# Kernel optimization log

Measured on AMD Instinct MI355X. Metric: run time of the kernel, lower is better.

## Reference

```python
import jax, jax.numpy as jnp
import numpy as np

N_CLASSES = 40
EMBED_DIM = 128
MOMENTUM = 0.1
LAMBDA_R, LAMBDA_C, LAMBDA_M = 1.0, 0.5, 1.0
BATCH = 262144


def setup_inputs() -> dict:
    key = jax.random.key(0)
    k1, k2, k3 = jax.random.split(key, 3)
    z = jax.random.normal(k1, (BATCH, EMBED_DIM), dtype=jnp.float32)
    y = jax.random.randint(k2, (BATCH,), 0, N_CLASSES)
    centers = jax.random.normal(k3, (N_CLASSES, EMBED_DIM), dtype=jnp.float32)
    initialized = jnp.ones((N_CLASSES,), dtype=bool)
    # buffers derived from class_counts (imbalanced ramp), r0=gamma=m0=1, alpha=0.25
    counts = jnp.asarray([1000.0 * (i + 1) for i in range(N_CLASSES)], jnp.float32)
    n_max = jnp.max(counts)
    target_radii = 1.0 + 1.0 * jnp.log(n_max / (counts + 1.0))
    margins = 1.0 * jnp.power(n_max / (counts + 1.0), 0.25)
    return {"z": z, "y": y, "centers": centers, "initialized": initialized,
            "target_radii": target_radii, "margins": margins}


def _update_centers(z, y, centers, initialized):
    # EMA centroid update on detached embeddings (torch.no_grad equivalent).
    zs = jax.lax.stop_gradient(z)
    sums = jax.ops.segment_sum(zs, y, num_segments=N_CLASSES)            # [C, D]
    cnt = jax.ops.segment_sum(jnp.ones((zs.shape[0],), zs.dtype), y,
                              num_segments=N_CLASSES)                    # [C]
    mean = sums / jnp.maximum(cnt, 1.0)[:, None]
    ema = (1.0 - MOMENTUM) * centers + MOMENTUM * mean
    new = jnp.where(initialized[:, None], ema, mean)                     # first-touch init
    return jnp.where((cnt > 0)[:, None], new, centers)                   # skip empty classes


def reference(z, y, centers, initialized, target_radii, margins):
    c = _update_centers(z, y, centers, initialized)                      # [C, D]

    # radial loss: smooth L1 (beta=1) between ||z|| and per-class target radius
    r = jnp.linalg.norm(z, axis=-1)                                      # [B]
    d = r - target_radii[y]
    ad = jnp.abs(d)
    loss_radial = jnp.mean(jnp.where(ad < 1.0, 0.5 * d * d, ad - 0.5))

    # compact loss: mean squared distance to own centroid
    diff = z - c[y]                                                      # [B, D]
    loss_compact = jnp.mean(jnp.sum(diff * diff, axis=-1))

    # margin loss: min distance to any other class centroid via Gram trick
    z2 = jnp.sum(z * z, axis=-1)                                         # [B]
    c2 = jnp.sum(c * c, axis=-1)                                         # [C]
    d2 = z2[:, None] + c2[None, :] - 2.0 * (z @ c.T)                     # [B, C]
    dist = jnp.sqrt(jnp.maximum(d2, 0.0))
    own = y[:, None] == jnp.arange(N_CLASSES)[None, :]                   # [B, C] bool
    dist_opp = jnp.min(jnp.where(own, jnp.inf, dist), axis=1)            # [B]
    loss_margin = jnp.mean(jax.nn.relu(margins[y] - dist_opp))

    return LAMBDA_R * loss_radial + LAMBDA_C * loss_compact + LAMBDA_M * loss_margin
```

## Files before the change

kernel.cpp:

```cpp
#include <hip/hip_runtime.h>
#include <math.h>

#define BATCH 262144
#define DIM   128
#define NCLS  40
#define NCP   48
#define CD    (NCLS * DIM)

#define TB1 512
#define NB1 256
#define TB3 256
#define NB3 (BATCH / 256)

typedef __attribute__((ext_vector_type(8))) short short8;
typedef __attribute__((ext_vector_type(4))) float f32x4;

__device__ __forceinline__ short f2bf(float f) {
    unsigned u = __float_as_uint(f);
    u += 0x7fffu + ((u >> 16) & 1u);
    return (short)(u >> 16);
}

#define K1_ALL(M) M(0) M(1) M(2) M(3) M(4) M(5) M(6) M(7) M(8) M(9) \
                  M(10) M(11) M(12) M(13) M(14) M(15) M(16) M(17) M(18) M(19) \
                  M(20) M(21) M(22) M(23) M(24) M(25) M(26) M(27) M(28) M(29) \
                  M(30) M(31) M(32) M(33) M(34) M(35) M(36) M(37) M(38) M(39)
#define K1_DECL(c) float a##c = 0.0f;
#define K1_CASE(c) case c: a##c += v; break;
#define K1_ST(c)   s_acc[w][(c) * 64 + lane] = a##c;

__global__ __launch_bounds__(TB1) void k1_segsum(const float* __restrict__ z,
                                                 const int* __restrict__ y,
                                                 float* __restrict__ ps,
                                                 float* __restrict__ gcnt) {
    __shared__ float s_acc[8][NCLS * 64];
    __shared__ float s_cnt[NCLS];
    const int t = threadIdx.x;
    if (t < NCLS) s_cnt[t] = 0.0f;
    __syncthreads();

    const int w    = t >> 6;
    const int lane = t & 63;
    const int p    = w >> 1;
    const int h    = w & 1;
    const int base = blockIdx.x * 1024;

    int yy[4];
#pragma unroll
    for (int g = 0; g < 4; ++g) yy[g] = y[base + 4 * (g * 64 + lane) + p];

    if (h == 0) {
#pragma unroll
        for (int g = 0; g < 4; ++g) atomicAdd(&s_cnt[yy[g]], 1.0f);
    }

    const float* __restrict__ zp = z + (size_t)base * DIM + h * 64 + lane;

    float vb[8];
#pragma unroll
    for (int q = 0; q < 8; ++q) vb[q] = zp[(size_t)(4 * q + p) * DIM];

    K1_ALL(K1_DECL)

#pragma unroll 1
    for (int g = 0; g < 4; ++g) {
        const int yg = yy[g];
#pragma unroll 1
        for (int j0 = 0; j0 < 64; j0 += 8) {
#pragma unroll
            for (int q = 0; q < 8; ++q) {
                const int sj = g * 64 + j0 + q;
                const float v = vb[q];
                int sn = sj + 8;
                if (sn > 255) sn = sj;
                vb[q] = zp[(size_t)(4 * sn + p) * DIM];
                const int cls = __builtin_amdgcn_readlane(yg, j0 + q);
                switch (cls) { K1_ALL(K1_CASE) default: break; }
            }
        }
    }

    K1_ALL(K1_ST)
    __syncthreads();

    float* __restrict__ ps_b = ps + (size_t)blockIdx.x * CD;
    for (int i = t; i < CD; i += TB1) {
        const int cls = i >> 7;
        const int d   = i & 127;
        const int hh  = d >> 6, dl = d & 63;
        float ssum = 0.0f;
#pragma unroll
        for (int pp = 0; pp < 4; ++pp) ssum += s_acc[(pp << 1) | hh][cls * 64 + dl];
        ps_b[i] = ssum;
    }
    if (t < NCLS) atomicAdd(&gcnt[t], s_cnt[t]);
}

__global__ __launch_bounds__(512) void k2_centers(const float* __restrict__ part_sums,
                                                  const float* __restrict__ gcnt,
                                                  const float* __restrict__ centers,
                                                  short* __restrict__ cbf,
                                                  float* __restrict__ c2_out) {
    const int j  = blockIdx.x;
    const int t  = threadIdx.x;
    const int d  = t & 127;
    const int qr = t >> 7;

    if (j >= NCLS) {
        if (qr == 0) cbf[j * DIM + d] = 0;
        if (t == 0) c2_out[j] = 1e30f;
        return;
    }

    const float* __restrict__ p = part_sums + j * DIM + d + (size_t)(qr * 64) * CD;
    float s = 0.0f;
#pragma unroll 8
    for (int b = 0; b < 64; ++b) s += p[(size_t)b * CD];

    __shared__ float red[512];
    red[t] = s;
    __syncthreads();

    float cv = 0.0f;
    if (qr == 0) {
        const float ssum = red[d] + red[d + 128] + red[d + 256] + red[d + 384];
        const float cnt  = gcnt[j];
        const float mean = ssum / fmaxf(cnt, 1.0f);
        const float ctr  = centers[j * DIM + d];
        const float ema  = 0.9f * ctr + 0.1f * mean;
        cv = (cnt > 0.0f) ? ema : ctr;
        cbf[j * DIM + d] = f2bf(cv);
    }
    __syncthreads();
    red[t] = cv * cv;
    __syncthreads();
    for (int off = 256; off > 0; off >>= 1) {
        if (t < off) red[t] += red[t + off];
        __syncthreads();
    }
    if (t == 0) c2_out[j] = red[0];
}

__global__ __launch_bounds__(TB3) void k3_loss(const float* __restrict__ z,
                                               const int* __restrict__ y,
                                               const short* __restrict__ cbf,
                                               const float* __restrict__ c2,
                                               const float* __restrict__ tr,
                                               const float* __restrict__ mg,
                                               float* __restrict__ out) {
    __shared__ float s_S[4][64 * 52];
    __shared__ float s_c2[NCP];

    const int t = threadIdx.x;
    if (t < NCP) s_c2[t] = c2[t];

    const int w    = t >> 6;
    const int lane = t & 63;
    const int q    = lane >> 4;
    const int col  = lane & 15;
    const int wavebase = blockIdx.x * 256 + w * 64;

    short8 bfrag[3][4];
#pragma unroll
    for (int ct = 0; ct < 3; ++ct)
#pragma unroll
        for (int s = 0; s < 4; ++s)
            bfrag[ct][s] = *(const short8*)(cbf + (ct * 16 + col) * DIM + s * 32 + q * 8);

    __syncthreads();

#pragma unroll 1
    for (int rt = 0; rt < 4; ++rt) {
        const float* __restrict__ zrow =
            z + (size_t)(wavebase + rt * 16 + col) * DIM + q * 8;

        float4 f[8];
#pragma unroll
        for (int s = 0; s < 4; ++s) {
            f[2 * s]     = *(const float4*)(zrow + s * 32);
            f[2 * s + 1] = *(const float4*)(zrow + s * 32 + 4);
        }

        float zp = 0.0f;
#pragma unroll
        for (int i = 0; i < 8; ++i) {
            zp = fmaf(f[i].x, f[i].x, zp);
            zp = fmaf(f[i].y, f[i].y, zp);
            zp = fmaf(f[i].z, f[i].z, zp);
            zp = fmaf(f[i].w, f[i].w, zp);
        }

        short8 afr[4];
#pragma unroll
        for (int s = 0; s < 4; ++s) {
            const float4 f0 = f[2 * s], f1 = f[2 * s + 1];
            afr[s][0] = f2bf(f0.x); afr[s][1] = f2bf(f0.y);
            afr[s][2] = f2bf(f0.z); afr[s][3] = f2bf(f0.w);
            afr[s][4] = f2bf(f1.x); afr[s][5] = f2bf(f1.y);
            afr[s][6] = f2bf(f1.z); afr[s][7] = f2bf(f1.w);
        }

        f32x4 acc0 = {0.f, 0.f, 0.f, 0.f};
        f32x4 acc1 = {0.f, 0.f, 0.f, 0.f};
        f32x4 acc2 = {0.f, 0.f, 0.f, 0.f};
#pragma unroll
        for (int s = 0; s < 4; ++s) {
            acc0 = __builtin_amdgcn_mfma_f32_16x16x32_bf16(afr[s], bfrag[0][s], acc0, 0, 0, 0);
            acc1 = __builtin_amdgcn_mfma_f32_16x16x32_bf16(afr[s], bfrag[1][s], acc1, 0, 0, 0);
            acc2 = __builtin_amdgcn_mfma_f32_16x16x32_bf16(afr[s], bfrag[2][s], acc2, 0, 0, 0);
        }

        zp += __shfl_xor(zp, 16);
        zp += __shfl_xor(zp, 32);
        if (q == 0) s_S[w][(rt * 16 + col) * 52 + 48] = zp;

#pragma unroll
        for (int reg = 0; reg < 4; ++reg) {
            const int rr = rt * 16 + q * 4 + reg;
            s_S[w][rr * 52 + col]      = acc0[reg];
            s_S[w][rr * 52 + 16 + col] = acc1[reg];
            s_S[w][rr * 52 + 32 + col] = acc2[reg];
        }
    }

    const int row = blockIdx.x * 256 + t;
    const int cls = y[row];
    const float z2v = s_S[w][lane * 52 + 48];

    float own_d2 = 0.0f;
    float mind2  = 3.4e38f;
#pragma unroll
    for (int k = 0; k < 12; ++k) {
        const float4 Sv = *(const float4*)&s_S[w][lane * 52 + 4 * k];
        const float Se[4] = {Sv.x, Sv.y, Sv.z, Sv.w};
#pragma unroll
        for (int e = 0; e < 4; ++e) {
            const int j = 4 * k + e;
            float d2 = fmaxf(z2v + s_c2[j] - 2.0f * Se[e], 0.0f);
            const bool isown = (j == cls);
            own_d2 = isown ? d2 : own_d2;
            mind2  = isown ? mind2 : fminf(mind2, d2);
        }
    }

    const float r  = sqrtf(z2v);
    const float dd = r - tr[cls];
    const float ad = fabsf(dd);
    const float rad = (ad < 1.0f) ? 0.5f * dd * dd : ad - 0.5f;

    const float dist = sqrtf(mind2);
    const float marg = fmaxf(mg[cls] - dist, 0.0f);

    const float tot = rad + 0.5f * own_d2 + marg;

    __syncthreads();
    float* s_red = &s_S[0][0];
    s_red[t] = tot;
    __syncthreads();
    for (int off = TB3 / 2; off > 0; off >>= 1) {
        if (t < off) s_red[t] += s_red[t + off];
        __syncthreads();
    }
    if (t == 0) atomicAdd(out, s_red[0] * (1.0f / (float)BATCH));
}

extern "C" void kernel_launch(void* const* d_in, const int* in_sizes, int n_in,
                              void* d_out, int out_size, void* d_ws, size_t ws_size,
                              hipStream_t stream) {
    const float* z       = (const float*)d_in[0];
    const int*   y       = (const int*)d_in[1];
    const float* centers = (const float*)d_in[2];
    const float* tr      = (const float*)d_in[4];
    const float* mg      = (const float*)d_in[5];
    float* out = (float*)d_out;

    float* ws        = (float*)d_ws;
    float* part_sums = ws;
    float* c2buf     = part_sums + (size_t)NB1 * CD;
    float* gcnt      = c2buf + NCP;
    short* cbf       = (short*)(gcnt + NCLS);

    hipMemsetAsync(gcnt, 0, NCLS * sizeof(float), stream);
    hipMemsetAsync(out, 0, sizeof(float), stream);

    k1_segsum<<<NB1, TB1, 0, stream>>>(z, y, part_sums, gcnt);
    k2_centers<<<NCP, 512, 0, stream>>>(part_sums, gcnt, centers, cbf, c2buf);
    k3_loss<<<NB3, TB3, 0, stream>>>(z, y, cbf, c2buf, tr, mg, out);
}
```

Measured before the change: 264.8 us.

## Restructure segment-sum kernel to 4 waves with float2 per-lane accumulators

The segment-sum kernel now uses 256 threads (4 waves) per block instead of 512. Each lane covers two adjacent dimensions with float2 loads and float2 register accumulators over 40 classes, and each wave walks 256 contiguous rows. The 8-slab shared-memory reduction is replaced by a single shared buffer that the waves accumulate into one after another, separated by barriers. The aim is to cut shared memory use and the final reduction cost, with wider coalesced loads. In exchange it doubles per-thread accumulator registers, which may hurt occupancy, and the serialized wave merges add barriers.

```diff
diff --git a/kernel.cpp b/kernel.cpp
--- a/kernel.cpp
+++ b/kernel.cpp
@@ -7,7 +7,7 @@
 #define NCP   48
 #define CD    (NCLS * DIM)
 
-#define TB1 512
+#define TB1 256
 #define NB1 256
 #define TB3 256
 #define NB3 (BATCH / 256)
@@ -25,74 +25,76 @@
                   M(10) M(11) M(12) M(13) M(14) M(15) M(16) M(17) M(18) M(19) \
                   M(20) M(21) M(22) M(23) M(24) M(25) M(26) M(27) M(28) M(29) \
                   M(30) M(31) M(32) M(33) M(34) M(35) M(36) M(37) M(38) M(39)
-#define K1_DECL(c) float a##c = 0.0f;
-#define K1_CASE(c) case c: a##c += v; break;
-#define K1_ST(c)   s_acc[w][(c) * 64 + lane] = a##c;
+#define K1_DECL(c) float2 a##c = {0.0f, 0.0f};
+#define K1_CASE(c) case c: a##c.x += v.x; a##c.y += v.y; break;
+#define K1_ST0(c)  s_buf[(c) * 64 + lane] = a##c;
+#define K1_RMW(c)  { float2 t_ = s_buf[(c) * 64 + lane];                     \
+                     t_.x += a##c.x; t_.y += a##c.y;                         \
+                     s_buf[(c) * 64 + lane] = t_; }
 
 __global__ __launch_bounds__(TB1) void k1_segsum(const float* __restrict__ z,
                                                  const int* __restrict__ y,
                                                  float* __restrict__ ps,
                                                  float* __restrict__ gcnt) {
-    __shared__ float s_acc[8][NCLS * 64];
-    __shared__ float s_cnt[NCLS];
+    __shared__ float2 s_buf[NCLS * 64];
+    __shared__ float  s_cnt[NCLS];
     const int t = threadIdx.x;
     if (t < NCLS) s_cnt[t] = 0.0f;
     __syncthreads();
 
-    const int w    = t >> 6;
-    const int lane = t & 63;
-    const int p    = w >> 1;
-    const int h    = w & 1;
-    const int base = blockIdx.x * 1024;
-
-    int yy[4];
-#pragma unroll
-    for (int g = 0; g < 4; ++g) yy[g] = y[base + 4 * (g * 64 + lane) + p];
-
-    if (h == 0) {
-#pragma unroll
-        for (int g = 0; g < 4; ++g) atomicAdd(&s_cnt[yy[g]], 1.0f);
-    }
-
-    const float* __restrict__ zp = z + (size_t)base * DIM + h * 64 + lane;
-
-    float vb[8];
-#pragma unroll
-    for (int q = 0; q < 8; ++q) vb[q] = zp[(size_t)(4 * q + p) * DIM];
+    const int w     = t >> 6;
+    const int lane  = t & 63;
+    const int rbase = blockIdx.x * 1024 + w * 256;
+
+    const int yA = y[rbase + lane];
+    const int yB = y[rbase + 64 + lane];
+    const int yC = y[rbase + 128 + lane];
+    const int yD = y[rbase + 192 + lane];
+    atomicAdd(&s_cnt[yA], 1.0f);
+    atomicAdd(&s_cnt[yB], 1.0f);
+    atomicAdd(&s_cnt[yC], 1.0f);
+    atomicAdd(&s_cnt[yD], 1.0f);
+
+    const float* __restrict__ zp = z + (size_t)rbase * DIM + lane * 2;
+
+    float2 vb[16];
+#pragma unroll
+    for (int q = 0; q < 16; ++q) vb[q] = *(const float2*)(zp + (size_t)q * DIM);
 
     K1_ALL(K1_DECL)
 
 #pragma unroll 1
-    for (int g = 0; g < 4; ++g) {
-        const int yg = yy[g];
+    for (int jj = 0; jj < 4; ++jj) {
+        int yj = yA;
+        if (jj == 1) yj = yB;
+        if (jj == 2) yj = yC;
+        if (jj == 3) yj = yD;
 #pragma unroll 1
-        for (int j0 = 0; j0 < 64; j0 += 8) {
-#pragma unroll
-            for (int q = 0; q < 8; ++q) {
-                const int sj = g * 64 + j0 + q;
-                const float v = vb[q];
-                int sn = sj + 8;
-                if (sn > 255) sn = sj;
-                vb[q] = zp[(size_t)(4 * sn + p) * DIM];
-                const int cls = __builtin_amdgcn_readlane(yg, j0 + q);
+        for (int i0 = 0; i0 < 64; i0 += 16) {
+#pragma unroll
+            for (int q = 0; q < 16; ++q) {
+                const int i = jj * 64 + i0 + q;
+                const float2 v = vb[q];
+                int sn = i + 16;
+                if (sn > 255) sn = i;
+                vb[q] = *(const float2*)(zp + (size_t)sn * DIM);
+                const int cls = __builtin_amdgcn_readlane(yj, i0 + q);
                 switch (cls) { K1_ALL(K1_CASE) default: break; }
             }
         }
     }
 
-    K1_ALL(K1_ST)
-    __syncthreads();
-
-    float* __restrict__ ps_b = ps + (size_t)blockIdx.x * CD;
-    for (int i = t; i < CD; i += TB1) {
-        const int cls = i >> 7;
-        const int d   = i & 127;
-        const int hh  = d >> 6, dl = d & 63;
-        float ssum = 0.0f;
-#pragma unroll
-        for (int pp = 0; pp < 4; ++pp) ssum += s_acc[(pp << 1) | hh][cls * 64 + dl];
-        ps_b[i] = ssum;
-    }
+    if (w == 0) { K1_ALL(K1_ST0) }
+    __syncthreads();
+    if (w == 1) { K1_ALL(K1_RMW) }
+    __syncthreads();
+    if (w == 2) { K1_ALL(K1_RMW) }
+    __syncthreads();
+    if (w == 3) { K1_ALL(K1_RMW) }
+    __syncthreads();
+
+    float2* __restrict__ psb = (float2*)(ps + (size_t)blockIdx.x * CD);
+    for (int i = t; i < NCLS * 64; i += TB1) psb[i] = s_buf[i];
     if (t < NCLS) atomicAdd(&gcnt[t], s_cnt[t]);
 }
 
```

Result: no change. 261.1 us (-1.4%).
